# Performance work log

Measured on AMD Instinct MI355X. Metric: run time of the kernel, lower is better.

## Reference

```python
import jax, jax.numpy as jnp
import numpy as np

V, D, H, L, F, S, HI, DI, TOPK = 50257, 1024, 16, 8, 4096, 1024, 4, 64, 512
DH = D // H
EPS = 1e-6


def rmsnorm(x, w):
    # matches torch: norm = ||x||_2 * D^-0.5 ; out = w * x / (norm + eps)
    n = jnp.linalg.norm(x, axis=-1, keepdims=True) * (x.shape[-1] ** -0.5)
    return w * (x / (n + EPS))


def setup_inputs() -> dict:
    key = jax.random.key(0)
    ks = jax.random.split(key, 16)
    std = 0.02
    tokens = jax.random.randint(ks[0], (2, S), 0, V)
    embed_w = jax.random.normal(ks[1], (V, D), jnp.float32) * std
    pos_w = jax.random.normal(ks[2], (S, D), jnp.float32) * std
    wq = jax.random.normal(ks[3], (L, D, D), jnp.float32) * std
    wk = jax.random.normal(ks[4], (L, D, D), jnp.float32) * std
    wv = jax.random.normal(ks[5], (L, D, D), jnp.float32) * std
    wo = jax.random.normal(ks[6], (L, D, D), jnp.float32) * std
    iq = jax.random.normal(ks[7], (L, D, HI * DI), jnp.float32) * std
    ik = jax.random.normal(ks[8], (L, D, DI), jnp.float32) * std
    iw = jax.random.normal(ks[9], (L, D, HI), jnp.float32) * std
    w1 = jax.random.normal(ks[10], (L, D, F), jnp.float32) * std
    w2 = jax.random.normal(ks[11], (L, F, D), jnp.float32) * std
    norm1 = jnp.ones((L, D), jnp.float32)
    norm2 = jnp.ones((L, D), jnp.float32)
    norm_f = jnp.ones((D,), jnp.float32)
    return dict(tokens=tokens, embed_w=embed_w, pos_w=pos_w, wq=wq, wk=wk,
                wv=wv, wo=wo, iq=iq, ik=ik, iw=iw, w1=w1, w2=w2,
                norm1=norm1, norm2=norm2, norm_f=norm_f)


def _block(x, p, causal):
    (wq, wk, wv, wo, iq, ik, iw, w1, w2, n1, n2) = p
    B = x.shape[0]
    NEG = jnp.finfo(x.dtype).min
    h = rmsnorm(x, n1)
    # --- lightning indexer: scores [B, S, S] ---
    qi = (h @ iq).reshape(B, S, HI, DI)          # [B,S,HI,DI]
    ki = h @ ik                                   # [B,S,DI]
    wt = h @ iw                                   # [B,S,HI]
    idx_logits = jax.nn.relu(jnp.einsum('bqhd,bkd->bhqk', qi, ki))
    idx_scores = jnp.einsum('bqh,bhqk->bqk', wt, idx_logits)  # [B,S,S]
    masked_idx = jnp.where(causal, idx_scores, NEG)
    _, top_i = jax.lax.top_k(masked_idx, TOPK)    # [B,S,TOPK]
    bi = jnp.arange(B)[:, None, None]
    qix = jnp.arange(S)[None, :, None]
    topk_mask = jnp.zeros((B, S, S), bool).at[bi, qix, top_i].set(True)
    allowed = causal & topk_mask                  # [B,S,S]
    # --- sparse multi-head attention (masked dense form, same math) ---
    q = (h @ wq).reshape(B, S, H, DH)
    k = (h @ wk).reshape(B, S, H, DH)
    v = (h @ wv).reshape(B, S, H, DH)
    att = jnp.einsum('bqhd,bkhd->bhqk', q, k) / jnp.sqrt(jnp.float32(DH))
    att = jnp.where(allowed[:, None, :, :], att, NEG)
    p_att = jax.nn.softmax(att, axis=-1)
    out = jnp.einsum('bhqk,bkhd->bqhd', p_att, v).reshape(B, S, D) @ wo
    x = x + out
    # --- feed-forward (exact GELU as nn.GELU) ---
    h2 = rmsnorm(x, n2)
    x = x + jax.nn.gelu(h2 @ w1, approximate=False) @ w2
    return x


def reference(tokens, embed_w, pos_w, wq, wk, wv, wo, iq, ik, iw, w1, w2,
              norm1, norm2, norm_f):
    x = embed_w[tokens] + pos_w[None, :tokens.shape[1], :]
    causal = jnp.tril(jnp.ones((S, S), bool))[None]  # [1,S,S]

    def step(x, p):
        return _block(x, p, causal), None

    x, _ = jax.lax.scan(step, x, (wq, wk, wv, wo, iq, ik, iw, w1, w2, norm1, norm2))
    x = rmsnorm(x, norm_f)
    logits = x @ embed_w.T  # tied lm_head
    return logits
```

## Files before the change

### kernel.cpp

```cpp
#include <hip/hip_runtime.h>
#include <cstdint>
#include <cstddef>

#define S_LEN 1024
#define D_DIM 1024
#define NH 16
#define DHD 64
#define NL 8
#define FF_DIM 4096
#define HI_N 4
#define DI_N 64
#define TOPK_N 512
#define BSROWS 2048
#define VOCAB 50257
#define VPAD 50304
#define NTILES_V 393
#define YPX 50

#define QKV_LD 3072
#define IDX_LD 384
#define COL_QI 0
#define COL_KI 256
#define COL_WT 320

#define NEGF -3.0e38f

typedef __attribute__((ext_vector_type(8))) _Float16 half8;
typedef __attribute__((ext_vector_type(4))) _Float16 half4v;
typedef __attribute__((ext_vector_type(4))) float f32x4;

#if __has_builtin(__builtin_amdgcn_mfma_f32_16x16x16f16)
#define MFMA16F(a, b, c) __builtin_amdgcn_mfma_f32_16x16x16f16((a), (b), (c), 0, 0, 0)
#else
static __device__ __forceinline__ f32x4 mfma16f_asm(half4v a, half4v b, f32x4 c) {
  f32x4 d;
  asm volatile("v_mfma_f32_16x16x16_f16 %0, %1, %2, %3\n\ts_nop 7\n\ts_nop 7"
               : "=v"(d) : "v"(a), "v"(b), "v"(c));
  return d;
}
#define MFMA16F(a, b, c) mfma16f_asm((a), (b), (c))
#endif

typedef const __attribute__((address_space(1))) void* gas_ptr;
typedef __attribute__((address_space(3))) void* las_ptr;
__device__ __forceinline__ void gload16(const void* g, void* l) {
#if __has_builtin(__builtin_amdgcn_global_load_lds)
  __builtin_amdgcn_global_load_lds((gas_ptr)g, (las_ptr)l, 16, 0, 0);
#else
  *(uint4*)l = *(const uint4*)g;
#endif
}

__device__ __forceinline__ short f2h(float x) {
  _Float16 h = (_Float16)x;
  return *reinterpret_cast<short*>(&h);
}
__device__ __forceinline__ float h2f(short b) {
  _Float16 h = *reinterpret_cast<_Float16*>(&b);
  return (float)h;
}
__device__ __forceinline__ void split_h(float x, short& hi, short& lo) {
  hi = f2h(x);
  lo = f2h(x - h2f(hi));
}

__global__ __launch_bounds__(256) void embed_kernel(
    const int* __restrict__ tokens, const float* __restrict__ E,
    const float* __restrict__ P, float* __restrict__ X)
{
  int bs = blockIdx.x;
  int s = bs & (S_LEN - 1);
  int tid = threadIdx.x;
  int tok = tokens[bs];
  float4 e = ((const float4*)(E + (size_t)tok * D_DIM))[tid];
  float4 p = ((const float4*)(P + (size_t)s * D_DIM))[tid];
  float4 o; o.x = e.x + p.x; o.y = e.y + p.y; o.z = e.z + p.z; o.w = e.w + p.w;
  ((float4*)(X + (size_t)bs * D_DIM))[tid] = o;
}

__global__ __launch_bounds__(256) void cvt_embed_kernel(
    const float* __restrict__ E, short* __restrict__ Eh)
{
  const long valid4 = (long)VOCAB * D_DIM / 4;
  const long total4 = (long)VPAD * D_DIM / 4;
  long i = (long)blockIdx.x * 256 + threadIdx.x;
  long stride = (long)gridDim.x * 256;
  for (; i < total4; i += stride) {
    short4 o = make_short4(0, 0, 0, 0);
    if (i < valid4) {
      float4 v = ((const float4*)E)[i];
      o = make_short4(f2h(v.x), f2h(v.y), f2h(v.z), f2h(v.w));
    }
    ((short4*)Eh)[i] = o;
  }
}

__global__ __launch_bounds__(256) void rmsnorm_split_kernel(
    const float* __restrict__ X, const float* __restrict__ W,
    short* __restrict__ O )
{
  int r = blockIdx.x;
  int tid = threadIdx.x;
  float4 v = ((const float4*)(X + (size_t)r * D_DIM))[tid];
  float ss = v.x * v.x + v.y * v.y + v.z * v.z + v.w * v.w;
  __shared__ float red[4];
  __shared__ float sh_inv;
  for (int o = 32; o; o >>= 1) ss += __shfl_down(ss, o);
  if ((tid & 63) == 0) red[tid >> 6] = ss;
  __syncthreads();
  if (tid == 0) {
    float s = red[0] + red[1] + red[2] + red[3];
    sh_inv = 1.0f / (sqrtf(s) * 0.03125f + 1e-6f);
  }
  __syncthreads();
  float inv = sh_inv;
  float4 w = ((const float4*)W)[tid];
  float o0 = w.x * v.x * inv, o1 = w.y * v.y * inv;
  float o2 = w.z * v.z * inv, o3 = w.w * v.w * inv;
  short4 hi, lo;
  split_h(o0, hi.x, lo.x); split_h(o1, hi.y, lo.y);
  split_h(o2, hi.z, lo.z); split_h(o3, hi.w, lo.w);
  ((short4*)(O + (size_t)r * D_DIM))[tid] = hi;
  ((short4*)(O + (size_t)BSROWS * D_DIM + (size_t)r * D_DIM))[tid] = lo;
}

__global__ __launch_bounds__(256) void rmsnorm_h_kernel(
    const float* __restrict__ X, const float* __restrict__ W, short* __restrict__ O)
{
  int r = blockIdx.x;
  int tid = threadIdx.x;
  float4 v = ((const float4*)(X + (size_t)r * D_DIM))[tid];
  float ss = v.x * v.x + v.y * v.y + v.z * v.z + v.w * v.w;
  __shared__ float red[4];
  __shared__ float sh_inv;
  for (int o = 32; o; o >>= 1) ss += __shfl_down(ss, o);
  if ((tid & 63) == 0) red[tid >> 6] = ss;
  __syncthreads();
  if (tid == 0) {
    float s = red[0] + red[1] + red[2] + red[3];
    sh_inv = 1.0f / (sqrtf(s) * 0.03125f + 1e-6f);
  }
  __syncthreads();
  float inv = sh_inv;
  float4 w = ((const float4*)W)[tid];
  short4 o4 = make_short4(f2h(w.x * v.x * inv), f2h(w.y * v.y * inv),
                          f2h(w.z * v.z * inv), f2h(w.w * v.w * inv));
  ((short4*)(O + (size_t)r * D_DIM))[tid] = o4;
}

__global__ __launch_bounds__(256) void packT_all_kernel(
    const float* __restrict__ W0, short* __restrict__ BT0, int K, int N)
{
  __shared__ float t[32][33];
  int z = blockIdx.z;
  const float* W = W0 + (size_t)z * K * N;
  short* BT = BT0 + (size_t)z * N * K;
  int n0 = blockIdx.x * 32, k0 = blockIdx.y * 32;
  int tx = threadIdx.x, ty = threadIdx.y;
#pragma unroll
  for (int r = 0; r < 32; r += 8)
    t[ty + r][tx] = W[(size_t)(k0 + ty + r) * N + n0 + tx];
  __syncthreads();
#pragma unroll
  for (int r = 0; r < 32; r += 8)
    BT[(size_t)(n0 + ty + r) * K + k0 + tx] = f2h(t[tx][ty + r]);
}

__global__ __launch_bounds__(256) void pack_qkv_all_kernel(
    const float* __restrict__ wq0, const float* __restrict__ wk0,
    const float* __restrict__ wv0, short* __restrict__ BT0)
{
  __shared__ float t[32][33];
  int z = blockIdx.z;
  const float* wq = wq0 + (size_t)z * D_DIM * D_DIM;
  const float* wk = wk0 + (size_t)z * D_DIM * D_DIM;
  const float* wv = wv0 + (size_t)z * D_DIM * D_DIM;
  short* BT = BT0 + (size_t)z * QKV_LD * D_DIM;
  int n0 = blockIdx.x * 32, k0 = blockIdx.y * 32;
  int tx = threadIdx.x, ty = threadIdx.y;
  const float* src = (n0 < 1024) ? wq : (n0 < 2048) ? wk : wv;
  int c0 = n0 & 1023;
#pragma unroll
  for (int r = 0; r < 32; r += 8)
    t[ty + r][tx] = src[(size_t)(k0 + ty + r) * 1024 + c0 + tx];
  __syncthreads();
#pragma unroll
  for (int r = 0; r < 32; r += 8)
    BT[(size_t)(n0 + ty + r) * D_DIM + k0 + tx] = f2h(t[tx][ty + r]);
}

__global__ __launch_bounds__(256) void pack_idx_all_kernel(
    const float* __restrict__ iq0, const float* __restrict__ ik0,
    const float* __restrict__ iw0, short* __restrict__ BT0)
{
  __shared__ float t[32][33];
  const size_t plane = (size_t)IDX_LD * D_DIM;
  int z = blockIdx.z;
  const float* iq = iq0 + (size_t)z * D_DIM * (HI_N * DI_N);
  const float* ik = ik0 + (size_t)z * D_DIM * DI_N;
  const float* iw = iw0 + (size_t)z * D_DIM * HI_N;
  short* BT = BT0 + (size_t)z * 2 * plane;
  int n0 = blockIdx.x * 32, k0 = blockIdx.y * 32;
  int tx = threadIdx.x, ty = threadIdx.y;
  const float* src = nullptr; int ld = 0, c0 = 0;
  if (n0 < 256)      { src = iq; ld = 256; c0 = n0; }
  else if (n0 < 320) { src = ik; ld = 64;  c0 = n0 - 256; }
  else if (n0 < 352) { src = iw; ld = 4;   c0 = n0 - 320; }
#pragma unroll
  for (int r = 0; r < 32; r += 8) {
    float v = 0.f;
    int c = c0 + tx;
    if (src && c < ld) v = src[(size_t)(k0 + ty + r) * ld + c];
    t[ty + r][tx] = v;
  }
  __syncthreads();
#pragma unroll
  for (int r = 0; r < 32; r += 8) {
    short hi, lo;
    split_h(t[tx][ty + r], hi, lo);
    size_t o = (size_t)(n0 + ty + r) * D_DIM + k0 + tx;
    BT[o] = hi;
    BT[plane + o] = lo;
  }
}

#define RA 40

__global__ __launch_bounds__(256) void gemm_split_kernel(
    const short* __restrict__ A, size_t aplane,
    const short* __restrict__ BT, size_t bplane,
    float* __restrict__ C, int M, int N, int K)
{
  __shared__ short Al[2 * 128 * RA];
  __shared__ short Bl[2 * 128 * RA];
  int tid = threadIdx.x;
  int wave = tid >> 6, lane = tid & 63;
  int wr = (wave >> 1) * 64, wc = (wave & 1) * 64;
  int lr = lane & 15, lk = lane >> 4;
  int m0 = blockIdx.y * 128, n0 = blockIdx.x * 128;
  f32x4 acc[4][4] = {};

  for (int k0 = 0; k0 < K; k0 += 32) {
    __syncthreads();
#pragma unroll
    for (int f = 0; f < 4; ++f) {
      int idx = tid + f * 256;
      int p = idx >> 9, r2 = idx & 511;
      int row = r2 >> 2, sub = r2 & 3;
      uint4 v = *(const uint4*)(A + (size_t)p * aplane + (size_t)(m0 + row) * K + k0 + sub * 8);
      *(uint4*)(Al + p * 128 * RA + row * RA + sub * 8) = v;
    }
#pragma unroll
    for (int f = 0; f < 4; ++f) {
      int idx = tid + f * 256;
      int p = idx >> 9, r2 = idx & 511;
      int row = r2 >> 2, sub = r2 & 3;
      uint4 v = *(const uint4*)(BT + (size_t)p * bplane + (size_t)(n0 + row) * K + k0 + sub * 8);
      *(uint4*)(Bl + p * 128 * RA + row * RA + sub * 8) = v;
    }
    __syncthreads();
    half8 ah[4], al[4], bh[4], bl[4];
#pragma unroll
    for (int i = 0; i < 4; ++i) {
      ah[i] = *(const half8*)(Al + (wr + i * 16 + lr) * RA + lk * 8);
      al[i] = *(const half8*)(Al + 128 * RA + (wr + i * 16 + lr) * RA + lk * 8);
    }
#pragma unroll
    for (int j = 0; j < 4; ++j) {
      bh[j] = *(const half8*)(Bl + (wc + j * 16 + lr) * RA + lk * 8);
      bl[j] = *(const half8*)(Bl + 128 * RA + (wc + j * 16 + lr) * RA + lk * 8);
    }
#pragma unroll
    for (int i = 0; i < 4; ++i)
#pragma unroll
      for (int j = 0; j < 4; ++j) {
        f32x4 a = acc[i][j];
        a = __builtin_amdgcn_mfma_f32_16x16x32_f16(al[i], bh[j], a, 0, 0, 0);
        a = __builtin_amdgcn_mfma_f32_16x16x32_f16(ah[i], bl[j], a, 0, 0, 0);
        a = __builtin_amdgcn_mfma_f32_16x16x32_f16(ah[i], bh[j], a, 0, 0, 0);
        acc[i][j] = a;
      }
  }
#pragma unroll
  for (int i = 0; i < 4; ++i)
#pragma unroll
    for (int r = 0; r < 4; ++r) {
      int m = m0 + wr + i * 16 + lk * 4 + r;
#pragma unroll
      for (int j = 0; j < 4; ++j) {
        int n = n0 + wc + j * 16 + lr;
        if (n < N) C[(size_t)m * N + n] = acc[i][j][r];
      }
    }
}

template<int BM, int EPI>
__global__ __launch_bounds__(256) void gemm_g_kernel(
    const short* __restrict__ A, const short* __restrict__ BT,
    const float* __restrict__ R, void* __restrict__ C, int M, int N, int K)
{
  constexpr int MI = BM / 32;
  __shared__ short Al[BM * 32];
  __shared__ short Bl[128 * 32];
  int tid = threadIdx.x;
  int wave = tid >> 6, lane = tid & 63;
  int wr = (wave >> 1) * (BM / 2), wc = (wave & 1) * 64;
  int lr = lane & 15, lk = lane >> 4;
  int m0 = blockIdx.y * BM, n0 = blockIdx.x * 128;
  f32x4 acc[MI][4] = {};

  for (int k0 = 0; k0 < K; k0 += 32) {
    __syncthreads();
#pragma unroll
    for (int f = 0; f < BM / 64; ++f) {
      int idx = tid + f * 256;
      gload16(A + (size_t)(m0 + (idx >> 2)) * K + k0 + (idx & 3) * 8, Al + idx * 8);
    }
#pragma unroll
    for (int f = 0; f < 2; ++f) {
      int idx = tid + f * 256;
      gload16(BT + (size_t)(n0 + (idx >> 2)) * K + k0 + (idx & 3) * 8, Bl + idx * 8);
    }
    __syncthreads();
    half8 af[MI], bfr[4];
#pragma unroll
    for (int i = 0; i < MI; ++i)
      af[i] = *(const half8*)(Al + (wr + i * 16 + lr) * 32 + lk * 8);
#pragma unroll
    for (int j = 0; j < 4; ++j)
      bfr[j] = *(const half8*)(Bl + (wc + j * 16 + lr) * 32 + lk * 8);
#pragma unroll
    for (int i = 0; i < MI; ++i)
#pragma unroll
      for (int j = 0; j < 4; ++j)
        acc[i][j] = __builtin_amdgcn_mfma_f32_16x16x32_f16(af[i], bfr[j], acc[i][j], 0, 0, 0);
  }
#pragma unroll
  for (int i = 0; i < MI; ++i)
#pragma unroll
    for (int r = 0; r < 4; ++r) {
      int m = m0 + wr + i * 16 + lk * 4 + r;
#pragma unroll
      for (int j = 0; j < 4; ++j) {
        int n = n0 + wc + j * 16 + lr;
        float v = acc[i][j][r];
        if (EPI == 1) {
          ((short*)C)[(size_t)m * N + n] = f2h(v);
        } else if (EPI == 2) {
          v = 0.5f * v * (1.0f + erff(v * 0.70710678118654752f));
          ((short*)C)[(size_t)m * N + n] = f2h(v);
        } else {
          ((float*)C)[(size_t)m * N + n] = v + R[(size_t)m * N + n];
        }
      }
    }
}

__global__ __launch_bounds__(256) void gemm_logits_g_kernel(
    const short* __restrict__ A, const short* __restrict__ BT,
    float* __restrict__ C, int M, int N, int K)
{
  int bid = blockIdx.x;
  int xcd = bid & 7, idx = bid >> 3;
  int mt = idx & 15, yt = (idx >> 4) + xcd * YPX;
  if (yt >= NTILES_V) return;
  int m0 = mt * 128, n0 = yt * 128;

  __shared__ short Al[128 * 32];
  __shared__ short Bl[128 * 32];
  int tid = threadIdx.x;
  int wave = tid >> 6, lane = tid & 63;
  int wr = (wave >> 1) * 64, wc = (wave & 1) * 64;
  int lr = lane & 15, lk = lane >> 4;
  f32x4 acc[4][4] = {};

  for (int k0 = 0; k0 < K; k0 += 32) {
    __syncthreads();
#pragma unroll
    for (int f = 0; f < 2; ++f) {
      int i2 = tid + f * 256;
      gload16(A + (size_t)(m0 + (i2 >> 2)) * K + k0 + (i2 & 3) * 8, Al + i2 * 8);
    }
#pragma unroll
    for (int f = 0; f < 2; ++f) {
      int i2 = tid + f * 256;
      gload16(BT + (size_t)(n0 + (i2 >> 2)) * K + k0 + (i2 & 3) * 8, Bl + i2 * 8);
    }
    __syncthreads();
    half8 af[4], bfr[4];
#pragma unroll
    for (int i = 0; i < 4; ++i)
      af[i] = *(const half8*)(Al + (wr + i * 16 + lr) * 32 + lk * 8);
#pragma unroll
    for (int j = 0; j < 4; ++j)
      bfr[j] = *(const half8*)(Bl + (wc + j * 16 + lr) * 32 + lk * 8);
#pragma unroll
    for (int i = 0; i < 4; ++i)
#pragma unroll
      for (int j = 0; j < 4; ++j)
        acc[i][j] = __builtin_amdgcn_mfma_f32_16x16x32_f16(af[i], bfr[j], acc[i][j], 0, 0, 0);
  }
#pragma unroll
  for (int i = 0; i < 4; ++i)
#pragma unroll
    for (int r = 0; r < 4; ++r) {
      int m = m0 + wr + i * 16 + lk * 4 + r;
#pragma unroll
      for (int j = 0; j < 4; ++j) {
        int n = n0 + wc + j * 16 + lr;
        if (n < N) C[(size_t)m * N + n] = acc[i][j][r];
      }
    }
}

__global__ __launch_bounds__(256) void gemm_logits_f32b_kernel(
    const short* __restrict__ A, const float* __restrict__ BT,
    float* __restrict__ C, int M, int N, int K)
{
  __shared__ short Al[128 * RA];
  __shared__ short Bl[128 * RA];
  int tid = threadIdx.x;
  int wave = tid >> 6, lane = tid & 63;
  int wr = (wave >> 1) * 64, wc = (wave & 1) * 64;
  int lr = lane & 15, lk = lane >> 4;
  int m0 = blockIdx.y * 128, n0 = blockIdx.x * 128;
  f32x4 acc[4][4] = {};

  for (int k0 = 0; k0 < K; k0 += 32) {
    __syncthreads();
#pragma unroll
    for (int f = 0; f < 2; ++f) {
      int idx = tid + f * 256, row = idx >> 2, sub = idx & 3;
      uint4 v = *(const uint4*)(A + (size_t)(m0 + row) * K + k0 + sub * 8);
      *(uint4*)(Al + row * RA + sub * 8) = v;
    }
#pragma unroll
    for (int f = 0; f < 4; ++f) {
      int idx = tid + f * 256, row = idx >> 3, qq = idx & 7;
      int gn = n0 + row;
      float4 v = make_float4(0.f, 0.f, 0.f, 0.f);
      if (gn < N) v = *(const float4*)(BT + (size_t)gn * K + k0 + qq * 4);
      *(short4*)(Bl + row * RA + qq * 4) =
          make_short4(f2h(v.x), f2h(v.y), f2h(v.z), f2h(v.w));
    }
    __syncthreads();
    half8 af[4], bfr[4];
#pragma unroll
    for (int i = 0; i < 4; ++i)
      af[i] = *(const half8*)(Al + (wr + i * 16 + lr) * RA + lk * 8);
#pragma unroll
    for (int j = 0; j < 4; ++j)
      bfr[j] = *(const half8*)(Bl + (wc + j * 16 + lr) * RA + lk * 8);
#pragma unroll
    for (int i = 0; i < 4; ++i)
#pragma unroll
      for (int j = 0; j < 4; ++j)
        acc[i][j] = __builtin_amdgcn_mfma_f32_16x16x32_f16(af[i], bfr[j], acc[i][j], 0, 0, 0);
  }
#pragma unroll
  for (int i = 0; i < 4; ++i)
#pragma unroll
    for (int r = 0; r < 4; ++r) {
      int m = m0 + wr + i * 16 + lk * 4 + r;
#pragma unroll
      for (int j = 0; j < 4; ++j) {
        int n = n0 + wc + j * 16 + lr;
        if (n < N) C[(size_t)m * N + n] = acc[i][j][r];
      }
    }
}

__device__ __forceinline__ unsigned int ford(float f) {
  unsigned int u = __float_as_uint(f);
  return (u & 0x80000000u) ? ~u : (u | 0x80000000u);
}

__global__ __launch_bounds__(256) void idx_topk_kernel(
    const float* __restrict__ Hx, unsigned int* __restrict__ MASK)
{
  int bq = blockIdx.x;
  int q = bq & (S_LEN - 1);
  int b = bq >> 10;
  int tid = threadIdx.x;
  int n = q + 1;
  if (n <= TOPK_N) {
    if (tid < 32) {
      int full = n >> 5, rem = n & 31;
      unsigned int w = 0u;
      if (tid < full) w = 0xFFFFFFFFu;
      else if (tid == full && rem) w = (1u << rem) - 1u;
      MASK[(size_t)bq * 32 + tid] = w;
    }
    return;
  }
  __shared__ float qi_s[HI_N * DI_N];
  __shared__ float wt_s[HI_N];
  __shared__ float sc[S_LEN];
  __shared__ unsigned long long keys[S_LEN];
  __shared__ unsigned int mw[32];
  qi_s[tid] = Hx[(size_t)bq * IDX_LD + COL_QI + tid];
  if (tid < HI_N) wt_s[tid] = Hx[(size_t)bq * IDX_LD + COL_WT + tid];
  __syncthreads();
  for (int k = tid; k < n; k += 256) {
    const float* kr = Hx + (size_t)(b * S_LEN + k) * IDX_LD + COL_KI;
    float d0 = 0.f, d1 = 0.f, d2 = 0.f, d3 = 0.f;
#pragma unroll
    for (int d = 0; d < DI_N; ++d) {
      float kv = kr[d];
      d0 = fmaf(qi_s[d], kv, d0);
      d1 = fmaf(qi_s[64 + d], kv, d1);
      d2 = fmaf(qi_s[128 + d], kv, d2);
      d3 = fmaf(qi_s[192 + d], kv, d3);
    }
    sc[k] = wt_s[0] * fmaxf(d0, 0.f) + wt_s[1] * fmaxf(d1, 0.f)
          + wt_s[2] * fmaxf(d2, 0.f) + wt_s[3] * fmaxf(d3, 0.f);
  }
  __syncthreads();
  for (int i = tid; i < S_LEN; i += 256) {
    unsigned long long kk = 0ull;
    if (i < n) kk = ((unsigned long long)ford(sc[i]) << 32) | (unsigned int)(S_LEN - 1 - i);
    keys[i] = kk;
  }
  __syncthreads();
  for (int size = 2; size <= S_LEN; size <<= 1) {
    for (int stride = size >> 1; stride > 0; stride >>= 1) {
      for (int t = tid; t < S_LEN / 2; t += 256) {
        int j = t & (stride - 1);
        int lo = ((t ^ j) << 1) | j;
        int hi = lo | stride;
        unsigned long long a = keys[lo], c = keys[hi];
        bool desc = ((lo & size) == 0);
        bool sw = desc ? (a < c) : (a > c);
        if (sw) { keys[lo] = c; keys[hi] = a; }
      }
      __syncthreads();
    }
  }
  if (tid < 32) mw[tid] = 0u;
  __syncthreads();
  for (int i = tid; i < TOPK_N; i += 256) {
    int k = S_LEN - 1 - (int)(keys[i] & 0xFFFFFFFFull);
    atomicOr(&mw[k >> 5], 1u << (k & 31));
  }
  __syncthreads();
  if (tid < 32) MASK[(size_t)bq * 32 + tid] = mw[tid];
}

__global__ __launch_bounds__(256) void attn_mfma_kernel(
    const short* __restrict__ QKV, const unsigned int* __restrict__ MASK,
    short* __restrict__ O )
{
  __shared__ unsigned int mlds[64 * 32];
  __shared__ short Kl[64 * 72];
  __shared__ short Vtl[64 * 68];
  int qt = blockIdx.x, h = blockIdx.y, b = blockIdx.z;
  int tid = threadIdx.x;
  int w = tid >> 6, l = tid & 63;
  int lq = l & 15, g = l >> 4;
  int q0 = qt * 64;

#pragma unroll
  for (int i = 0; i < 8; ++i) {
    int idx = tid + i * 256;
    mlds[idx] = MASK[((size_t)(b * S_LEN + q0 + (idx >> 5))) * 32 + (idx & 31)];
  }
  half4v qf[4];
  {
    const short* qrow = QKV + ((size_t)(b * S_LEN + q0 + w * 16 + lq)) * QKV_LD + h * DHD;
#pragma unroll
    for (int dt = 0; dt < 4; ++dt)
      qf[dt] = *(const half4v*)(qrow + dt * 16 + g * 4);
  }
  f32x4 acc_o[4] = {};
  float m_run = -1.0e30f, l_run = 0.f;
  const short* Kb = QKV + (size_t)b * S_LEN * QKV_LD + 1024 + h * DHD;
  const short* Vb = QKV + (size_t)b * S_LEN * QKV_LD + 2048 + h * DHD;
  const int mrow = w * 16 + lq;

  for (int kt = 0; kt <= qt; ++kt) {
    __syncthreads();
#pragma unroll
    for (int i = 0; i < 2; ++i) {
      int idx = tid + i * 256;
      int row = idx >> 3, sub = idx & 7;
      uint4 v = *(const uint4*)(Kb + (size_t)(kt * 64 + row) * QKV_LD + sub * 8);
      *(uint4*)(Kl + row * 72 + sub * 8) = v;
    }
    {
      int u = tid >> 1, half = tid & 1;
      int kg = u >> 3, dg = u & 7;
      int krow = kt * 64 + kg * 4 + half * 2;
      uint4 v0 = *(const uint4*)(Vb + (size_t)krow * QKV_LD + dg * 8);
      uint4 v1 = *(const uint4*)(Vb + (size_t)(krow + 1) * QKV_LD + dg * 8);
      const short* s0 = (const short*)&v0;
      const short* s1 = (const short*)&v1;
#pragma unroll
      for (int j = 0; j < 8; ++j)
        *(short2*)(Vtl + (dg * 8 + j) * 68 + kg * 4 + half * 2) = make_short2(s0[j], s1[j]);
    }
    __syncthreads();
    f32x4 s[4] = {};
#pragma unroll
    for (int dt = 0; dt < 4; ++dt)
#pragma unroll
      for (int ks = 0; ks < 4; ++ks) {
        half4v kf = *(const half4v*)(Kl + (ks * 16 + lq) * 72 + dt * 16 + g * 4);
        s[ks] = MFMA16F(kf, qf[dt], s[ks]);
      }
    float mx = NEGF;
#pragma unroll
    for (int ks = 0; ks < 4; ++ks) {
      int kbase = kt * 64 + ks * 16 + g * 4;
      unsigned mwv = mlds[mrow * 32 + (kbase >> 5)];
#pragma unroll
      for (int r = 0; r < 4; ++r) {
        float sv = ((mwv >> ((kbase + r) & 31)) & 1u) ? s[ks][r] * 0.125f : NEGF;
        s[ks][r] = sv;
        mx = fmaxf(mx, sv);
      }
    }
    mx = fmaxf(mx, __shfl_xor(mx, 16));
    mx = fmaxf(mx, __shfl_xor(mx, 32));
    float m_new = fmaxf(m_run, mx);
    float scale = __expf(m_run - m_new);
    float lsum = 0.f;
    half4v pf[4];
#pragma unroll
    for (int ks = 0; ks < 4; ++ks) {
      half4v t;
#pragma unroll
      for (int r = 0; r < 4; ++r) {
        float p = __expf(s[ks][r] - m_new);
        lsum += p;
        t[r] = (_Float16)p;
      }
      pf[ks] = t;
    }
    lsum += __shfl_xor(lsum, 16);
    lsum += __shfl_xor(lsum, 32);
    l_run = l_run * scale + lsum;
    m_run = m_new;
    float sc[4];
#pragma unroll
    for (int r = 0; r < 4; ++r) sc[r] = __shfl(scale, g * 4 + r);
#pragma unroll
    for (int dt = 0; dt < 4; ++dt) {
      f32x4 a = acc_o[dt];
      a[0] *= sc[0]; a[1] *= sc[1]; a[2] *= sc[2]; a[3] *= sc[3];
#pragma unroll
      for (int ks = 0; ks < 4; ++ks) {
        half4v vf = *(const half4v*)(Vtl + (dt * 16 + lq) * 68 + ks * 16 + g * 4);
        a = MFMA16F(pf[ks], vf, a);
      }
      acc_o[dt] = a;
    }
  }
  float linv[4];
#pragma unroll
  for (int r = 0; r < 4; ++r) linv[r] = 1.0f / __shfl(l_run, g * 4 + r);
#pragma unroll
  for (int dt = 0; dt < 4; ++dt)
#pragma unroll
    for (int r = 0; r < 4; ++r) {
      int q = q0 + w * 16 + g * 4 + r;
      float o = acc_o[dt][r] * linv[r];
      O[(size_t)(b * S_LEN + q) * D_DIM + h * DHD + dt * 16 + lq] = f2h(o);
    }
}

extern "C" void kernel_launch(void* const* d_in, const int* in_sizes, int n_in,
                              void* d_out, int out_size, void* d_ws, size_t ws_size,
                              hipStream_t stream) {
  (void)in_sizes; (void)n_in; (void)out_size;
  const int*   tokens  = (const int*)d_in[0];
  const float* embed_w = (const float*)d_in[1];
  const float* pos_w   = (const float*)d_in[2];
  const float* wq      = (const float*)d_in[3];
  const float* wk      = (const float*)d_in[4];
  const float* wv      = (const float*)d_in[5];
  const float* wo      = (const float*)d_in[6];
  const float* iqw     = (const float*)d_in[7];
  const float* ikw     = (const float*)d_in[8];
  const float* iww     = (const float*)d_in[9];
  const float* w1      = (const float*)d_in[10];
  const float* w2      = (const float*)d_in[11];
  const float* n1      = (const float*)d_in[12];
  const float* n2      = (const float*)d_in[13];
  const float* nf      = (const float*)d_in[14];
  float* logits = (float*)d_out;

  short* Hh = (short*)d_ws;
  size_t need_eh = ((size_t)BSROWS * D_DIM + (size_t)VPAD * D_DIM) * 2;
  bool use_eh = ws_size >= need_eh;
  short* Eh = Hh + (size_t)BSROWS * D_DIM;

  char* base = (char*)d_out;
  size_t off = (size_t)BSROWS * D_DIM * 4;
  float* X = logits;
  float* Hx = (float*)(base + off);    off += (size_t)BSROWS * IDX_LD * 4;
  short* QKVh = (short*)(base + off);  off += (size_t)BSROWS * QKV_LD * 2;
  short* Hsp = (short*)(base + off);   off += (size_t)2 * BSROWS * D_DIM * 2;
  short* AOh = (short*)(base + off);   off += (size_t)BSROWS * D_DIM * 2;
  short* FFh = (short*)(base + off);   off += (size_t)BSROWS * FF_DIM * 2;
  unsigned int* MASKb = (unsigned int*)(base + off); off += (size_t)BSROWS * 32 * 4;
  short* BTqkvA = (short*)(base + off); off += (size_t)NL * QKV_LD * D_DIM * 2;
  short* BTidxA = (short*)(base + off); off += (size_t)NL * 2 * IDX_LD * D_DIM * 2;
  short* BTwoA = (short*)(base + off);  off += (size_t)NL * D_DIM * D_DIM * 2;
  short* BTw1A = (short*)(base + off);  off += (size_t)NL * FF_DIM * D_DIM * 2;
  short* BTw2A = (short*)(base + off);  off += (size_t)NL * FF_DIM * D_DIM * 2;

  const size_t plH  = (size_t)BSROWS * D_DIM;
  const size_t plIx = (size_t)IDX_LD * D_DIM;

  hipLaunchKernelGGL(embed_kernel, dim3(BSROWS), dim3(256), 0, stream,
                     tokens, embed_w, pos_w, X);
  if (use_eh)
    hipLaunchKernelGGL(cvt_embed_kernel, dim3(8192), dim3(256), 0, stream, embed_w, Eh);

  hipLaunchKernelGGL(pack_qkv_all_kernel, dim3(QKV_LD / 32, 32, NL), dim3(32, 8), 0, stream,
                     wq, wk, wv, BTqkvA);
  hipLaunchKernelGGL(pack_idx_all_kernel, dim3(IDX_LD / 32, 32, NL), dim3(32, 8), 0, stream,
                     iqw, ikw, iww, BTidxA);
  hipLaunchKernelGGL(packT_all_kernel, dim3(32, 32, NL), dim3(32, 8), 0, stream,
                     wo, BTwoA, D_DIM, D_DIM);
  hipLaunchKernelGGL(packT_all_kernel, dim3(FF_DIM / 32, 32, NL), dim3(32, 8), 0, stream,
                     w1, BTw1A, D_DIM, FF_DIM);
  hipLaunchKernelGGL(packT_all_kernel, dim3(D_DIM / 32, FF_DIM / 32, NL), dim3(32, 8), 0, stream,
                     w2, BTw2A, FF_DIM, D_DIM);

  for (int l = 0; l < NL; ++l) {
    short* BTqkv = BTqkvA + (size_t)l * QKV_LD * D_DIM;
    short* BTidx = BTidxA + (size_t)l * 2 * IDX_LD * D_DIM;
    short* BTwo  = BTwoA + (size_t)l * D_DIM * D_DIM;
    short* BTw1  = BTw1A + (size_t)l * FF_DIM * D_DIM;
    short* BTw2  = BTw2A + (size_t)l * FF_DIM * D_DIM;

    hipLaunchKernelGGL(rmsnorm_split_kernel, dim3(BSROWS), dim3(256), 0, stream,
                       X, n1 + (size_t)l * D_DIM, Hsp);
    hipLaunchKernelGGL((gemm_g_kernel<128, 1>), dim3(QKV_LD / 128, 16), dim3(256), 0, stream,
                       Hsp, BTqkv, nullptr, QKVh, BSROWS, QKV_LD, D_DIM);
    hipLaunchKernelGGL(gemm_split_kernel, dim3(IDX_LD / 128, 16), dim3(256), 0, stream,
                       Hsp, plH, BTidx, plIx, Hx, BSROWS, IDX_LD, D_DIM);
    hipLaunchKernelGGL(idx_topk_kernel, dim3(BSROWS), dim3(256), 0, stream, Hx, MASKb);
    hipLaunchKernelGGL(attn_mfma_kernel, dim3(S_LEN / 64, NH, 2), dim3(256), 0, stream,
                       QKVh, MASKb, AOh);
    hipLaunchKernelGGL((gemm_g_kernel<64, 3>), dim3(8, 32), dim3(256), 0, stream,
                       AOh, BTwo, X, X, BSROWS, D_DIM, D_DIM);
    hipLaunchKernelGGL(rmsnorm_h_kernel, dim3(BSROWS), dim3(256), 0, stream,
                       X, n2 + (size_t)l * D_DIM, Hsp);
    hipLaunchKernelGGL((gemm_g_kernel<128, 2>), dim3(FF_DIM / 128, 16), dim3(256), 0, stream,
                       Hsp, BTw1, nullptr, FFh, BSROWS, FF_DIM, D_DIM);
    hipLaunchKernelGGL((gemm_g_kernel<64, 3>), dim3(8, 32), dim3(256), 0, stream,
                       FFh, BTw2, X, X, BSROWS, D_DIM, FF_DIM);
  }

  hipLaunchKernelGGL(rmsnorm_h_kernel, dim3(BSROWS), dim3(256), 0, stream, X, nf, Hh);
  if (use_eh) {
    hipLaunchKernelGGL(gemm_logits_g_kernel, dim3(8 * YPX * 16), dim3(256), 0, stream,
                       Hh, Eh, logits, BSROWS, VOCAB, D_DIM);
  } else {
    hipLaunchKernelGGL(gemm_logits_f32b_kernel, dim3((VOCAB + 127) / 128, 16), dim3(256), 0, stream,
                       Hh, embed_w, logits, BSROWS, VOCAB, D_DIM);
  }
}
```

Before: 3.691 ms.

## Double-buffer attention K/V tiles with async loads and shrink indexer GEMM tile

The attention kernel now double-buffers its K and V tiles in shared memory. It prefetches the next tile's K with gload16 into an XOR-swizzled unpadded layout and holds the next V rows in registers while computing the current tile. QK^T switches to the 16x16x32 MFMA with half8 fragments, and s_setprio raises wave priority around the MFMA sections. The indexer split GEMM is templated on block rows and launched with 64-row tiles, doubling its grid to fill more CUs. The costs are more LDS and register pressure and dependence on the gload16 helper and the swizzle being correct.

```diff
diff --git a/kernel.cpp b/kernel.cpp
--- a/kernel.cpp
+++ b/kernel.cpp
@@ -226,29 +226,31 @@
 
 #define RA 40
 
+template<int BM>
 __global__ __launch_bounds__(256) void gemm_split_kernel(
     const short* __restrict__ A, size_t aplane,
     const short* __restrict__ BT, size_t bplane,
     float* __restrict__ C, int M, int N, int K)
 {
-  __shared__ short Al[2 * 128 * RA];
+  constexpr int MI = BM / 32;
+  __shared__ short Al[2 * BM * RA];
   __shared__ short Bl[2 * 128 * RA];
   int tid = threadIdx.x;
   int wave = tid >> 6, lane = tid & 63;
-  int wr = (wave >> 1) * 64, wc = (wave & 1) * 64;
+  int wr = (wave >> 1) * (BM / 2), wc = (wave & 1) * 64;
   int lr = lane & 15, lk = lane >> 4;
-  int m0 = blockIdx.y * 128, n0 = blockIdx.x * 128;
-  f32x4 acc[4][4] = {};
+  int m0 = blockIdx.y * BM, n0 = blockIdx.x * 128;
+  f32x4 acc[MI][4] = {};
 
   for (int k0 = 0; k0 < K; k0 += 32) {
     __syncthreads();
 #pragma unroll
-    for (int f = 0; f < 4; ++f) {
+    for (int f = 0; f < BM / 32; ++f) {
       int idx = tid + f * 256;
-      int p = idx >> 9, r2 = idx & 511;
+      int p = idx / (BM * 4), r2 = idx % (BM * 4);
       int row = r2 >> 2, sub = r2 & 3;
       uint4 v = *(const uint4*)(A + (size_t)p * aplane + (size_t)(m0 + row) * K + k0 + sub * 8);
-      *(uint4*)(Al + p * 128 * RA + row * RA + sub * 8) = v;
+      *(uint4*)(Al + p * BM * RA + row * RA + sub * 8) = v;
     }
 #pragma unroll
     for (int f = 0; f < 4; ++f) {
@@ -259,30 +261,30 @@
       *(uint4*)(Bl + p * 128 * RA + row * RA + sub * 8) = v;
     }
     __syncthreads();
-    half8 ah[4], al[4], bh[4], bl[4];
-#pragma unroll
-    for (int i = 0; i < 4; ++i) {
+    half8 ah[MI], al_[MI], bh[4], bl_[4];
+#pragma unroll
+    for (int i = 0; i < MI; ++i) {
       ah[i] = *(const half8*)(Al + (wr + i * 16 + lr) * RA + lk * 8);
-      al[i] = *(const half8*)(Al + 128 * RA + (wr + i * 16 + lr) * RA + lk * 8);
+      al_[i] = *(const half8*)(Al + BM * RA + (wr + i * 16 + lr) * RA + lk * 8);
     }
 #pragma unroll
     for (int j = 0; j < 4; ++j) {
       bh[j] = *(const half8*)(Bl + (wc + j * 16 + lr) * RA + lk * 8);
-      bl[j] = *(const half8*)(Bl + 128 * RA + (wc + j * 16 + lr) * RA + lk * 8);
-    }
-#pragma unroll
-    for (int i = 0; i < 4; ++i)
+      bl_[j] = *(const half8*)(Bl + 128 * RA + (wc + j * 16 + lr) * RA + lk * 8);
+    }
+#pragma unroll
+    for (int i = 0; i < MI; ++i)
 #pragma unroll
       for (int j = 0; j < 4; ++j) {
         f32x4 a = acc[i][j];
-        a = __builtin_amdgcn_mfma_f32_16x16x32_f16(al[i], bh[j], a, 0, 0, 0);
-        a = __builtin_amdgcn_mfma_f32_16x16x32_f16(ah[i], bl[j], a, 0, 0, 0);
+        a = __builtin_amdgcn_mfma_f32_16x16x32_f16(al_[i], bh[j], a, 0, 0, 0);
+        a = __builtin_amdgcn_mfma_f32_16x16x32_f16(ah[i], bl_[j], a, 0, 0, 0);
         a = __builtin_amdgcn_mfma_f32_16x16x32_f16(ah[i], bh[j], a, 0, 0, 0);
         acc[i][j] = a;
       }
   }
 #pragma unroll
-  for (int i = 0; i < 4; ++i)
+  for (int i = 0; i < MI; ++i)
 #pragma unroll
     for (int r = 0; r < 4; ++r) {
       int m = m0 + wr + i * 16 + lk * 4 + r;
@@ -551,62 +553,76 @@
     short* __restrict__ O )
 {
   __shared__ unsigned int mlds[64 * 32];
-  __shared__ short Kl[64 * 72];
-  __shared__ short Vtl[64 * 68];
+  __shared__ short Kl[2][64 * 64];
+  __shared__ short Vtl[2][64 * 68];
   int qt = blockIdx.x, h = blockIdx.y, b = blockIdx.z;
   int tid = threadIdx.x;
   int w = tid >> 6, l = tid & 63;
   int lq = l & 15, g = l >> 4;
   int q0 = qt * 64;
+  const short* Kb = QKV + (size_t)b * S_LEN * QKV_LD + 1024 + h * DHD;
+  const short* Vb = QKV + (size_t)b * S_LEN * QKV_LD + 2048 + h * DHD;
+  int vu = tid >> 1, vhalf = tid & 1, vkg = vu >> 3, vdg = vu & 7;
 
 #pragma unroll
   for (int i = 0; i < 8; ++i) {
     int idx = tid + i * 256;
     mlds[idx] = MASK[((size_t)(b * S_LEN + q0 + (idx >> 5))) * 32 + (idx & 31)];
   }
-  half4v qf[4];
+  half8 qf[2];
   {
     const short* qrow = QKV + ((size_t)(b * S_LEN + q0 + w * 16 + lq)) * QKV_LD + h * DHD;
-#pragma unroll
-    for (int dt = 0; dt < 4; ++dt)
-      qf[dt] = *(const half4v*)(qrow + dt * 16 + g * 4);
-  }
-  f32x4 acc_o[4] = {};
-  float m_run = -1.0e30f, l_run = 0.f;
-  const short* Kb = QKV + (size_t)b * S_LEN * QKV_LD + 1024 + h * DHD;
-  const short* Vb = QKV + (size_t)b * S_LEN * QKV_LD + 2048 + h * DHD;
-  const int mrow = w * 16 + lq;
-
-  for (int kt = 0; kt <= qt; ++kt) {
-    __syncthreads();
+    qf[0] = *(const half8*)(qrow + g * 8);
+    qf[1] = *(const half8*)(qrow + 32 + g * 8);
+  }
+  {
 #pragma unroll
     for (int i = 0; i < 2; ++i) {
       int idx = tid + i * 256;
       int row = idx >> 3, sub = idx & 7;
-      uint4 v = *(const uint4*)(Kb + (size_t)(kt * 64 + row) * QKV_LD + sub * 8);
-      *(uint4*)(Kl + row * 72 + sub * 8) = v;
-    }
-    {
-      int u = tid >> 1, half = tid & 1;
-      int kg = u >> 3, dg = u & 7;
-      int krow = kt * 64 + kg * 4 + half * 2;
-      uint4 v0 = *(const uint4*)(Vb + (size_t)krow * QKV_LD + dg * 8);
-      uint4 v1 = *(const uint4*)(Vb + (size_t)(krow + 1) * QKV_LD + dg * 8);
-      const short* s0 = (const short*)&v0;
-      const short* s1 = (const short*)&v1;
-#pragma unroll
-      for (int j = 0; j < 8; ++j)
-        *(short2*)(Vtl + (dg * 8 + j) * 68 + kg * 4 + half * 2) = make_short2(s0[j], s1[j]);
-    }
-    __syncthreads();
+      gload16(Kb + (size_t)row * QKV_LD + (size_t)((sub ^ (row & 7)) * 8), &Kl[0][idx * 8]);
+    }
+    int krow = vkg * 4 + vhalf * 2;
+    uint4 v0 = *(const uint4*)(Vb + (size_t)krow * QKV_LD + vdg * 8);
+    uint4 v1 = *(const uint4*)(Vb + (size_t)(krow + 1) * QKV_LD + vdg * 8);
+    const short* s0 = (const short*)&v0;
+    const short* s1 = (const short*)&v1;
+#pragma unroll
+    for (int j = 0; j < 8; ++j)
+      *(short2*)(&Vtl[0][(vdg * 8 + j) * 68 + vkg * 4 + vhalf * 2]) = make_short2(s0[j], s1[j]);
+  }
+  __syncthreads();
+
+  f32x4 acc_o[4] = {};
+  float m_run = -1.0e30f, l_run = 0.f;
+  const int mrow = w * 16 + lq;
+  int cur = 0;
+
+  for (int kt = 0; kt <= qt; ++kt) {
+    bool more = kt < qt;
+    uint4 v0, v1;
+    if (more) {
+#pragma unroll
+      for (int i = 0; i < 2; ++i) {
+        int idx = tid + i * 256;
+        int row = idx >> 3, sub = idx & 7;
+        gload16(Kb + (size_t)((kt + 1) * 64 + row) * QKV_LD + (size_t)((sub ^ (row & 7)) * 8),
+                &Kl[cur ^ 1][idx * 8]);
+      }
+      int krow = (kt + 1) * 64 + vkg * 4 + vhalf * 2;
+      v0 = *(const uint4*)(Vb + (size_t)krow * QKV_LD + vdg * 8);
+      v1 = *(const uint4*)(Vb + (size_t)(krow + 1) * QKV_LD + vdg * 8);
+    }
     f32x4 s[4] = {};
-#pragma unroll
-    for (int dt = 0; dt < 4; ++dt)
-#pragma unroll
-      for (int ks = 0; ks < 4; ++ks) {
-        half4v kf = *(const half4v*)(Kl + (ks * 16 + lq) * 72 + dt * 16 + g * 4);
-        s[ks] = MFMA16F(kf, qf[dt], s[ks]);
-      }
+    __builtin_amdgcn_s_setprio(1);
+#pragma unroll
+    for (int ks = 0; ks < 4; ++ks) {
+      half8 kf0 = *(const half8*)(&Kl[cur][(ks * 16 + lq) * 64 + ((g ^ (lq & 7)) * 8)]);
+      half8 kf1 = *(const half8*)(&Kl[cur][(ks * 16 + lq) * 64 + (((4 + g) ^ (lq & 7)) * 8)]);
+      s[ks] = __builtin_amdgcn_mfma_f32_16x16x32_f16(kf0, qf[0], s[ks], 0, 0, 0);
+      s[ks] = __builtin_amdgcn_mfma_f32_16x16x32_f16(kf1, qf[1], s[ks], 0, 0, 0);
+    }
+    __builtin_amdgcn_s_setprio(0);
     float mx = NEGF;
 #pragma unroll
     for (int ks = 0; ks < 4; ++ks) {
@@ -643,17 +659,28 @@
     float sc[4];
 #pragma unroll
     for (int r = 0; r < 4; ++r) sc[r] = __shfl(scale, g * 4 + r);
+    __builtin_amdgcn_s_setprio(1);
 #pragma unroll
     for (int dt = 0; dt < 4; ++dt) {
       f32x4 a = acc_o[dt];
       a[0] *= sc[0]; a[1] *= sc[1]; a[2] *= sc[2]; a[3] *= sc[3];
 #pragma unroll
       for (int ks = 0; ks < 4; ++ks) {
-        half4v vf = *(const half4v*)(Vtl + (dt * 16 + lq) * 68 + ks * 16 + g * 4);
+        half4v vf = *(const half4v*)(&Vtl[cur][(dt * 16 + lq) * 68 + ks * 16 + g * 4]);
         a = MFMA16F(pf[ks], vf, a);
       }
       acc_o[dt] = a;
     }
+    __builtin_amdgcn_s_setprio(0);
+    if (more) {
+      const short* s0 = (const short*)&v0;
+      const short* s1 = (const short*)&v1;
+#pragma unroll
+      for (int j = 0; j < 8; ++j)
+        *(short2*)(&Vtl[cur ^ 1][(vdg * 8 + j) * 68 + vkg * 4 + vhalf * 2]) = make_short2(s0[j], s1[j]);
+    }
+    __syncthreads();
+    cur ^= 1;
   }
   float linv[4];
 #pragma unroll
@@ -739,7 +766,7 @@
                        X, n1 + (size_t)l * D_DIM, Hsp);
     hipLaunchKernelGGL((gemm_g_kernel<128, 1>), dim3(QKV_LD / 128, 16), dim3(256), 0, stream,
                        Hsp, BTqkv, nullptr, QKVh, BSROWS, QKV_LD, D_DIM);
-    hipLaunchKernelGGL(gemm_split_kernel, dim3(IDX_LD / 128, 16), dim3(256), 0, stream,
+    hipLaunchKernelGGL((gemm_split_kernel<64>), dim3(IDX_LD / 128, 32), dim3(256), 0, stream,
                        Hsp, plH, BTidx, plIx, Hx, BSROWS, IDX_LD, D_DIM);
     hipLaunchKernelGGL(idx_topk_kernel, dim3(BSROWS), dim3(256), 0, stream, Hx, MASKb);
     hipLaunchKernelGGL(attn_mfma_kernel, dim3(S_LEN / 64, NH, 2), dim3(256), 0, stream,
```

Result: no change. 3.631 ms (-1.6%).
